# Optimization experiments

Hardware: AMD Instinct MI355X
Metric: run time of the kernel (lower is better)

The kernel has to match this reference:

```python
import jax, jax.numpy as jnp
import numpy as np

N, D, L = 1000, 256, 7  # nodes, feature dim, layers (hardcoded in the torch module)
B = 64


def setup_inputs() -> dict:
    key = jax.random.key(0)
    ks = jax.random.split(key, 8)
    x = jax.random.normal(ks[0], (B, N, D), dtype=jnp.float32)
    # binary adjacency mask (diagonal is forced to 1 inside reference, as in torch)
    adj = (jax.random.uniform(ks[1], (B, N, N)) < 0.05).astype(jnp.float32)
    # stacked per-layer weights; torch Linear convention: y = x @ W.T + b
    W_attn = jax.random.normal(ks[2], (L, D, D), dtype=jnp.float32) * 0.01
    b_attn = jnp.zeros((L, D), jnp.float32)
    W0 = jax.random.normal(ks[3], (L, D, D), dtype=jnp.float32) * 0.05
    b0 = jnp.zeros((L, D), jnp.float32)
    W1 = jax.random.normal(ks[4], (L, D, D), dtype=jnp.float32) * 0.05
    b1 = jnp.zeros((L, D), jnp.float32)
    Wf = jax.random.normal(ks[5], (D, D), dtype=jnp.float32) * 0.05
    bf = jnp.zeros((D,), jnp.float32)
    return {"x": x, "adj": adj, "W_attn": W_attn, "b_attn": b_attn,
            "W0": W0, "b0": b0, "W1": W1, "b1": b1, "Wf": Wf, "bf": bf}


def reference(x, adj, W_attn, b_attn, W0, b0, W1, b1, Wf, bf):
    idx = jnp.arange(N)
    adj = adj.at[:, idx, idx].set(1.0)              # self-loops forced on
    eps_eye = (1e-5 * jnp.eye(N, dtype=x.dtype))    # added before masking
    for l in range(L):
        x0 = x
        q = x @ W_attn[l].T + b_attn[l]             # [B,N,D]
        s = jax.nn.sigmoid(jnp.einsum('bid,bjd->bij', q, x))  # [B,N,N]
        s = (s + eps_eye) * adj                     # mask by adjacency
        s = s / jnp.sum(s, axis=-1, keepdims=True)  # row-sum normalize
        x = jnp.einsum('bij,bjd->bid', s, x)        # weighted aggregate
        x = jax.nn.relu(x @ W0[l].T + b0[l])
        x = jax.nn.relu(x @ W1[l].T + b1[l])
        x = x + x0                                  # residual
    return x @ Wf.T + bf
```

## Files before the change

kernel.cpp:

```cpp
#include <hip/hip_runtime.h>
#include <hip/hip_bf16.h>

#define B_ 64
#define N_ 1000
#define NP 1024
#define D_ 256
#define L_ 7
#define MP (B_*NP)
#define PKB 262144

typedef unsigned short u16;
typedef __attribute__((ext_vector_type(4))) float f32x4;
typedef __bf16 bf16x8 __attribute__((ext_vector_type(8)));

static __device__ __forceinline__ u16 f2bf(float f) {
  __hip_bfloat16 h = __float2bfloat16(f);
  return *reinterpret_cast<u16*>(&h);
}
static __device__ __forceinline__ float bf2f(u16 u) {
  __hip_bfloat16 h;
  *reinterpret_cast<u16*>(&h) = u;
  return __bfloat162float(h);
}

static __device__ __forceinline__ void gl_lds16(const u16* g, u16* l) {
  __builtin_amdgcn_global_load_lds(
      (const __attribute__((address_space(1))) void*)g,
      (__attribute__((address_space(3))) void*)l, 16, 0, 0);
}

__global__ __launch_bounds__(64) void pack_mask_k(const float* __restrict__ adj,
                                                  unsigned long long* __restrict__ mask) {
  int row = blockIdx.x;
  int b = row / N_, i = row - b * N_;
  int lane = threadIdx.x;
  const float* arow = adj + (size_t)(b * N_ + i) * N_;
  #pragma unroll
  for (int j0 = 0; j0 < NP; j0 += 64) {
    int j = j0 + lane;
    bool on = (j < N_) && (arow[j] != 0.0f || j == i);
    unsigned long long m = __ballot(on);
    if (lane == 0) mask[((size_t)(b * NP + i)) * 16 + (j0 >> 6)] = m;
  }
}

__global__ __launch_bounds__(256) void conv_w_k(const float* __restrict__ Wa,
                                                const float* __restrict__ W0,
                                                const float* __restrict__ W1,
                                                const float* __restrict__ Wf,
                                                u16* __restrict__ wpk) {
  int T = blockIdx.x * 256 + threadIdx.x;
  const int NW = 3 * L_ + 1;
  if (T >= NW * 128 * 64) return;
  int lane = T & 63;
  int fid = T >> 6;
  int k = fid & 7, f = (fid >> 3) & 3, by = (fid >> 5) & 3, w = fid >> 7;
  const float* src;
  if (w < L_) src = Wa + (size_t)w * D_ * D_;
  else if (w < 2 * L_) src = W0 + (size_t)(w - L_) * D_ * D_;
  else if (w < 3 * L_) src = W1 + (size_t)(w - 2 * L_) * D_ * D_;
  else src = Wf;
  int row = by * 64 + f * 16 + (lane & 15);
  int col = k * 32 + ((lane >> 4) << 3);
  const float* s = src + (size_t)row * D_ + col;
  u16 out8[8];
  #pragma unroll
  for (int e = 0; e < 8; e++) out8[e] = f2bf(s[e]);
  *reinterpret_cast<bf16x8*>(wpk + (size_t)T * 8) =
      *reinterpret_cast<bf16x8*>(out8);
}

__global__ __launch_bounds__(256) void prep_x_k(const float* __restrict__ x,
                                                float* __restrict__ xc,
                                                u16* __restrict__ xb) {
  size_t t = (size_t)blockIdx.x * blockDim.x + threadIdx.x;
  const size_t total = (size_t)B_ * N_ * D_;
  if (t < total) {
    int b = (int)(t / (N_ * D_));
    int rem = (int)(t - (size_t)b * (N_ * D_));
    size_t o = (size_t)b * NP * D_ + rem;
    float v = x[t];
    xc[o] = v;
    xb[o] = f2bf(v);
  }
  const size_t padTotal = (size_t)B_ * (NP - N_) * D_;
  if (t < padTotal) {
    int b = (int)(t / ((NP - N_) * D_));
    int rem = (int)(t - (size_t)b * ((NP - N_) * D_));
    size_t o = (size_t)b * NP * D_ + (size_t)N_ * D_ + rem;
    xc[o] = 0.f;
    xb[o] = 0;
  }
}

__global__ __launch_bounds__(256) void pack_both_k(const u16* __restrict__ xb,
                                                   u16* __restrict__ xpk,
                                                   u16* __restrict__ pvpk) {
  __shared__ u16 t[64][65];
  int b = blockIdx.z;
  int cc = blockIdx.x;
  int bd = blockIdx.y;
  int i0 = cc * 64, d0 = bd * 64;
  int tid = threadIdx.x;
  int tx = tid & 63, ty = tid >> 6;
  const u16* src = xb + (size_t)b * NP * D_;
  #pragma unroll
  for (int r = ty; r < 64; r += 4)
    t[r][tx] = src[(size_t)(i0 + r) * D_ + d0 + tx];
  __syncthreads();
  int lane = tid & 63, q = tid >> 6;
  int l4 = lane >> 4, l15 = lane & 15;
  int dh = bd >> 1, dcb = (bd & 1) * 4;
  u16* dstp = pvpk + (size_t)b * PKB;
  #pragma unroll
  for (int kk = 0; kk < 2; kk++) {
    int frag = cc * 32 + dh * 16 + (dcb + q) * 2 + kk;
    bf16x8 v;
    #pragma unroll
    for (int e = 0; e < 8; e++)
      v[e] = *reinterpret_cast<const __bf16*>(&t[kk * 32 + (l4 << 3) + e][q * 16 + l15]);
    *reinterpret_cast<bf16x8*>(dstp + (size_t)frag * 512 + lane * 8) = v;
  }
  u16* dstq = xpk + (size_t)b * PKB;
  #pragma unroll
  for (int kk = 0; kk < 2; kk++) {
    int frag = cc * 32 + q * 8 + (2 * bd + kk);
    bf16x8 v;
    #pragma unroll
    for (int e = 0; e < 8; e++)
      v[e] = *reinterpret_cast<const __bf16*>(&t[l15 + 16 * q][kk * 32 + (l4 << 3) + e]);
    *reinterpret_cast<bf16x8*>(dstq + (size_t)frag * 512 + lane * 8) = v;
  }
}

template <int MODE, int APK>
__global__ __launch_bounds__(256) void linear_k(const u16* __restrict__ A,
                                                const u16* __restrict__ W,
                                                const float* __restrict__ bias,
                                                u16* __restrict__ outb,
                                                float* __restrict__ xc,
                                                u16* __restrict__ xbp,
                                                float* __restrict__ outf) {
  int lane = threadIdx.x & 63;
  int wv = threadIdx.x >> 6;
  int rbase = blockIdx.x * 64 + wv * 16;
  int cbase = blockIdx.y * 64;
  f32x4 acc[4] = {};
  const u16* Ar;
  if (APK) Ar = A + ((size_t)(rbase >> 4) << 12) + lane * 8;
  else     Ar = A + (size_t)(rbase + (lane & 15)) * D_ + ((lane >> 4) << 3);
  const u16* Wr = W + (size_t)blockIdx.y * (32 * 512) + lane * 8;
  #pragma unroll
  for (int k = 0; k < 8; k++) {
    bf16x8 a = APK ? *reinterpret_cast<const bf16x8*>(Ar + k * 512)
                   : *reinterpret_cast<const bf16x8*>(Ar + k * 32);
    #pragma unroll
    for (int f = 0; f < 4; f++) {
      bf16x8 bb = *reinterpret_cast<const bf16x8*>(Wr + (f * 8 + k) * 512);
      acc[f] = __builtin_amdgcn_mfma_f32_16x16x32_bf16(a, bb, acc[f], 0, 0, 0);
    }
  }
  int r0 = rbase + ((lane >> 4) << 2);
  int col = cbase + (lane & 15);
  #pragma unroll
  for (int f = 0; f < 4; f++) {
    int c = col + f * 16;
    float bv = bias[c];
    #pragma unroll
    for (int r = 0; r < 4; r++) {
      int row = r0 + r;
      float v = acc[f][r] + bv;
      if (MODE == 3) {
        int b = row >> 10, i = row & (NP - 1);
        if (i < N_) outf[((size_t)b * N_ + i) * D_ + c] = v;
      } else {
        size_t dst = ((size_t)(row >> 4) << 12) + ((c >> 5) << 9) +
                     ((((c >> 3) & 3) * 16 + (row & 15)) << 3) + (c & 7);
        outb[dst] = f2bf(v);
      }
    }
  }
}

template <int FINAL>
__global__ __launch_bounds__(256) void mlp_fused_k(const u16* __restrict__ A,
                                                   const u16* __restrict__ W0p,
                                                   const float* __restrict__ bias0,
                                                   const u16* __restrict__ W1p,
                                                   const float* __restrict__ bias1,
                                                   u16* __restrict__ xpk,
                                                   float* __restrict__ xc,
                                                   u16* __restrict__ pvpk,
                                                   const u16* __restrict__ Wqp,
                                                   const float* __restrict__ biasq,
                                                   u16* __restrict__ qpk,
                                                   float* __restrict__ outf) {
  __shared__ u16 h0lds[8192];
  __shared__ u16 xnlds[8192];
  int blk = blockIdx.x;
  int lane = threadIdx.x & 63;
  int wv = threadIdx.x >> 6;
  int rsub = wv & 1, ch = wv >> 1;
  int l15 = lane & 15, l4 = lane >> 4;

  const u16* Ar = A + (size_t)(blk * 32 + rsub * 16 + l15) * D_ + (l4 << 3);
  const u16* w0b = W0p + (size_t)(ch * 64) * 512 + lane * 8;
  #pragma unroll
  for (int hf = 0; hf < 2; hf++) {
    f32x4 acc1[4] = {};
    __builtin_amdgcn_s_setprio(1);
    #pragma unroll
    for (int k = 0; k < 8; k++) {
      bf16x8 a = *reinterpret_cast<const bf16x8*>(Ar + k * 32);
      #pragma unroll
      for (int ff = 0; ff < 4; ff++) {
        bf16x8 bb = *reinterpret_cast<const bf16x8*>(
            w0b + (hf * 32 + ff * 8 + k) * 512);
        acc1[ff] = __builtin_amdgcn_mfma_f32_16x16x32_bf16(a, bb, acc1[ff], 0, 0, 0);
      }
    }
    __builtin_amdgcn_s_setprio(0);
    #pragma unroll
    for (int ff = 0; ff < 4; ff++) {
      int fc = hf * 4 + ff;
      int c = ch * 128 + fc * 16 + l15;
      float bv = bias0[c];
      int base = rsub * 4096 + (ch * 4 + (fc >> 1)) * 512 +
                 (((fc * 2 + (l15 >> 3)) & 3) * 16 + l4 * 4) * 8 + (l15 & 7);
      #pragma unroll
      for (int r = 0; r < 4; r++)
        h0lds[base + r * 8] = f2bf(fmaxf(acc1[ff][r] + bv, 0.f));
    }
  }
  __syncthreads();

  const u16* w1b = W1p + (size_t)(ch * 64) * 512 + lane * 8;
  int r0g = blk * 32 + rsub * 16 + l4 * 4;
  #pragma unroll
  for (int hf = 0; hf < 2; hf++) {
    f32x4 acc2[4] = {};
    __builtin_amdgcn_s_setprio(1);
    #pragma unroll
    for (int k = 0; k < 8; k++) {
      bf16x8 a = *reinterpret_cast<const bf16x8*>(&h0lds[rsub * 4096 + k * 512 + lane * 8]);
      #pragma unroll
      for (int ff = 0; ff < 4; ff++) {
        bf16x8 bb = *reinterpret_cast<const bf16x8*>(
            w1b + (hf * 32 + ff * 8 + k) * 512);
        acc2[ff] = __builtin_amdgcn_mfma_f32_16x16x32_bf16(a, bb, acc2[ff], 0, 0, 0);
      }
    }
    __builtin_amdgcn_s_setprio(0);
    #pragma unroll
    for (int ff = 0; ff < 4; ff++) {
      int fc = hf * 4 + ff;
      int c = ch * 128 + fc * 16 + l15;
      float bv = bias1[c];
      int base = rsub * 4096 + (ch * 4 + (fc >> 1)) * 512 +
                 (((fc * 2 + (l15 >> 3)) & 3) * 16 + l4 * 4) * 8 + (l15 & 7);
      #pragma unroll
      for (int r = 0; r < 4; r++) {
        int row = r0g + r;
        float v = fmaxf(acc2[ff][r] + bv, 0.f);
        size_t o = (size_t)row * D_ + c;
        float nv = v + xc[o];
        if (!FINAL) xc[o] = nv;
        xnlds[base + r * 8] = f2bf(nv);
      }
    }
  }
  __syncthreads();

  if (!FINAL) {
    int tid = threadIdx.x;
    u16* dst = xpk + ((size_t)blk << 13) + tid * 8;
    #pragma unroll
    for (int i = 0; i < 4; i++)
      *reinterpret_cast<bf16x8*>(dst + i * 2048) =
          *reinterpret_cast<const bf16x8*>(&xnlds[tid * 8 + i * 2048]);
    int rg = tid & 3;
    int cb = tid >> 2;
    int bb2 = blk >> 5;
    int fp_base = ((blk & 31) >> 1) * 32 + (blk & 1);
    #pragma unroll
    for (int pass = 0; pass < 4; pass++) {
      int c = pass * 64 + cb;
      int fragp = fp_base + (c >> 7) * 16 + ((c >> 4) & 7) * 2;
      size_t dp = (size_t)bb2 * PKB + (size_t)fragp * 512 +
                  (size_t)((rg * 16 + (c & 15)) << 3);
      int xoff = (rg >> 1) * 4096 + (c >> 5) * 512 +
                 ((((c >> 3) & 3) * 16 + (rg & 1) * 8) << 3) + (c & 7);
      u16 v[8];
      #pragma unroll
      for (int j = 0; j < 8; j++) v[j] = xnlds[xoff + j * 8];
      *reinterpret_cast<bf16x8*>(pvpk + dp) = *reinterpret_cast<bf16x8*>(v);
    }
  }

  const u16* wqb = Wqp + (size_t)(ch * 64) * 512 + lane * 8;
  #pragma unroll
  for (int hf = 0; hf < 2; hf++) {
    f32x4 acc3[4] = {};
    __builtin_amdgcn_s_setprio(1);
    #pragma unroll
    for (int k = 0; k < 8; k++) {
      bf16x8 a = *reinterpret_cast<const bf16x8*>(&xnlds[rsub * 4096 + k * 512 + lane * 8]);
      #pragma unroll
      for (int ff = 0; ff < 4; ff++) {
        bf16x8 bb = *reinterpret_cast<const bf16x8*>(
            wqb + (hf * 32 + ff * 8 + k) * 512);
        acc3[ff] = __builtin_amdgcn_mfma_f32_16x16x32_bf16(a, bb, acc3[ff], 0, 0, 0);
      }
    }
    __builtin_amdgcn_s_setprio(0);
    #pragma unroll
    for (int ff = 0; ff < 4; ff++) {
      int fc = hf * 4 + ff;
      int c = ch * 128 + fc * 16 + l15;
      float bv = biasq[c];
      #pragma unroll
      for (int r = 0; r < 4; r++) {
        int row = r0g + r;
        float v = acc3[ff][r] + bv;
        if (FINAL) {
          int b = row >> 10, i = row & (NP - 1);
          if (i < N_) outf[((size_t)b * N_ + i) * D_ + c] = v;
        } else {
          size_t dst = ((size_t)(row >> 4) << 12) + ((c >> 5) << 9) +
                       ((((c >> 3) & 3) * 16 + (row & 15)) << 3) + (c & 7);
          qpk[dst] = f2bf(v);
        }
      }
    }
  }
}

__global__ __launch_bounds__(512) void attn_fused_k(const u16* __restrict__ qpk,
                                                    const u16* __restrict__ xpk,
                                                    const u16* __restrict__ pvpk,
                                                    const unsigned long long* __restrict__ mask,
                                                    u16* __restrict__ yb) {
  __shared__ u16 xlds[16384];
  __shared__ u16 plds[2][64][64];
  __shared__ u16 qlds[16384];
  float* dlds = (float*)xlds;
  int wg = blockIdx.x;
  int xcd = wg & 7, slot = wg >> 3;
  int b = xcd * 8 + (slot >> 4);
  int rb = slot & 15;
  int rbase = rb * 64;
  int lane = threadIdx.x & 63;
  int wv = threadIdx.x >> 6;
  int rsub = wv & 3, jh = wv >> 2;
  int l15 = lane & 15, l4 = lane >> 4;
  int rowL = rsub * 16 + l4 * 4;

  const u16* xpkC = xpk + (size_t)b * PKB;
  const u16* pvkB = pvpk + (size_t)b * PKB + (size_t)((wv >> 2) * 16 + (wv & 3) * 4) * 512 + lane * 8;
  const unsigned long long* mB = mask + (size_t)b * (NP * 16);
  int swr = (l15 & 7) << 3;
  int pc0 = (l4 << 3) ^ swr;
  int pc1 = (32 | (l4 << 3)) ^ swr;

  f32x4 yacc[4][2] = {};
  float denp[4] = {0.f, 0.f, 0.f, 0.f};

  {
    const u16* gs = xpkC + wv * 2048 + lane * 8;
    u16* ld = &xlds[wv * 2048];
    #pragma unroll
    for (int i = 0; i < 4; i++)
      gl_lds16(gs + i * 512, ld + i * 512);
    const u16* gq = qpk + ((((size_t)b * NP + rbase) >> 4) << 12) + wv * 2048 + lane * 8;
    u16* lq = &qlds[wv * 2048];
    #pragma unroll
    for (int i = 0; i < 4; i++)
      gl_lds16(gq + i * 512, lq + i * 512);
  }
  __syncthreads();

  #pragma unroll 1
  for (int t = 0; t < 16; t++) {
    int pb = t & 1, pr = pb ^ 1;
    f32x4 sacc[2] = {};
    __builtin_amdgcn_s_setprio(1);
    #pragma unroll
    for (int k = 0; k < 8; k++) {
      bf16x8 a = *reinterpret_cast<const bf16x8*>(&qlds[rsub * 4096 + k * 512 + lane * 8]);
      bf16x8 b0 = *reinterpret_cast<const bf16x8*>(&xlds[((jh * 2) * 8 + k) * 512 + lane * 8]);
      sacc[0] = __builtin_amdgcn_mfma_f32_16x16x32_bf16(a, b0, sacc[0], 0, 0, 0);
      bf16x8 b1 = *reinterpret_cast<const bf16x8*>(&xlds[((jh * 2 + 1) * 8 + k) * 512 + lane * 8]);
      sacc[1] = __builtin_amdgcn_mfma_f32_16x16x32_bf16(a, b1, sacc[1], 0, 0, 0);
    }
    __builtin_amdgcn_s_setprio(0);
    __syncthreads();
    if (t < 15) {
      const u16* gs = xpkC + (size_t)(t + 1) * 16384 + wv * 2048 + lane * 8;
      u16* ld = &xlds[wv * 2048];
      #pragma unroll
      for (int i = 0; i < 4; i++)
        gl_lds16(gs + i * 512, ld + i * 512);
    }
    #pragma unroll
    for (int r = 0; r < 4; r++) {
      int i = rbase + rowL + r;
      unsigned long long mw = (i < N_) ? mB[((size_t)i << 4) + t] : 0ull;
      int swz = ((rowL + r) & 7) << 3;
      #pragma unroll
      for (int fl = 0; fl < 2; fl++) {
        int jloc = jh * 32 + fl * 16 + l15;
        int j = t * 64 + jloc;
        float w = 0.f;
        if ((mw >> jloc) & 1ull) {
          float s = __builtin_amdgcn_rcpf(1.f + __expf(-sacc[fl][r]));
          w = s + (i == j ? 1e-5f : 0.f);
        }
        u16 wq = f2bf(w);
        plds[pb][rowL + r][jloc ^ swz] = wq;
        denp[r] += bf2f(wq);
      }
    }
    if (t > 0) {
      const u16* pvc = pvkB + (size_t)(t - 1) * (32 * 512);
      bf16x8 w00 = *reinterpret_cast<const bf16x8*>(pvc);
      bf16x8 w01 = *reinterpret_cast<const bf16x8*>(pvc + 512);
      bf16x8 w10 = *reinterpret_cast<const bf16x8*>(pvc + 1024);
      bf16x8 w11 = *reinterpret_cast<const bf16x8*>(pvc + 1536);
      __builtin_amdgcn_s_setprio(1);
      #pragma unroll
      for (int rt = 0; rt < 4; rt++) {
        bf16x8 ap0 = *reinterpret_cast<const bf16x8*>(&plds[pr][rt * 16 + l15][pc0]);
        yacc[rt][0] = __builtin_amdgcn_mfma_f32_16x16x32_bf16(ap0, w00, yacc[rt][0], 0, 0, 0);
        yacc[rt][1] = __builtin_amdgcn_mfma_f32_16x16x32_bf16(ap0, w10, yacc[rt][1], 0, 0, 0);
        bf16x8 ap1 = *reinterpret_cast<const bf16x8*>(&plds[pr][rt * 16 + l15][pc1]);
        yacc[rt][0] = __builtin_amdgcn_mfma_f32_16x16x32_bf16(ap1, w01, yacc[rt][0], 0, 0, 0);
        yacc[rt][1] = __builtin_amdgcn_mfma_f32_16x16x32_bf16(ap1, w11, yacc[rt][1], 0, 0, 0);
      }
      __builtin_amdgcn_s_setprio(0);
    }
    __syncthreads();
  }

  {
    const u16* pvc = pvkB + (size_t)15 * (32 * 512);
    bf16x8 w00 = *reinterpret_cast<const bf16x8*>(pvc);
    bf16x8 w01 = *reinterpret_cast<const bf16x8*>(pvc + 512);
    bf16x8 w10 = *reinterpret_cast<const bf16x8*>(pvc + 1024);
    bf16x8 w11 = *reinterpret_cast<const bf16x8*>(pvc + 1536);
    __builtin_amdgcn_s_setprio(1);
    #pragma unroll
    for (int rt = 0; rt < 4; rt++) {
      bf16x8 ap0 = *reinterpret_cast<const bf16x8*>(&plds[1][rt * 16 + l15][pc0]);
      yacc[rt][0] = __builtin_amdgcn_mfma_f32_16x16x32_bf16(ap0, w00, yacc[rt][0], 0, 0, 0);
      yacc[rt][1] = __builtin_amdgcn_mfma_f32_16x16x32_bf16(ap0, w10, yacc[rt][1], 0, 0, 0);
      bf16x8 ap1 = *reinterpret_cast<const bf16x8*>(&plds[1][rt * 16 + l15][pc1]);
      yacc[rt][0] = __builtin_amdgcn_mfma_f32_16x16x32_bf16(ap1, w01, yacc[rt][0], 0, 0, 0);
      yacc[rt][1] = __builtin_amdgcn_mfma_f32_16x16x32_bf16(ap1, w11, yacc[rt][1], 0, 0, 0);
    }
    __builtin_amdgcn_s_setprio(0);
  }

  __syncthreads();
  #pragma unroll
  for (int r = 0; r < 4; r++) {
    float d = denp[r];
    #pragma unroll
    for (int m = 1; m < 16; m <<= 1) d += __shfl_xor(d, m, 64);
    if (l15 == 0) dlds[wv * 16 + l4 * 4 + r] = d;
  }
  __syncthreads();
  u16* yB = yb + ((size_t)b * NP + rbase) * D_ + wv * 32 + l15;
  #pragma unroll
  for (int rt = 0; rt < 4; rt++) {
    #pragma unroll
    for (int r = 0; r < 4; r++) {
      int rl = rt * 16 + l4 * 4 + r;
      int i = rbase + rl;
      float den = dlds[rt * 16 + l4 * 4 + r] + dlds[(rt + 4) * 16 + l4 * 4 + r];
      float inv = (i < N_ && den > 0.f) ? 1.f / den : 0.f;
      #pragma unroll
      for (int ct = 0; ct < 2; ct++)
        yB[(size_t)rl * D_ + ct * 16] = f2bf(yacc[rt][ct][r] * inv);
    }
  }
}

extern "C" void kernel_launch(void* const* d_in, const int* in_sizes, int n_in,
                              void* d_out, int out_size, void* d_ws, size_t ws_size,
                              hipStream_t stream) {
  const float* x   = (const float*)d_in[0];
  const float* adj = (const float*)d_in[1];
  const float* Wa  = (const float*)d_in[2];
  const float* ba  = (const float*)d_in[3];
  const float* W0  = (const float*)d_in[4];
  const float* b0_ = (const float*)d_in[5];
  const float* W1  = (const float*)d_in[6];
  const float* b1_ = (const float*)d_in[7];
  const float* Wf  = (const float*)d_in[8];
  const float* bff = (const float*)d_in[9];
  float* out = (float*)d_out;

  char* p = (char*)d_ws;
  auto alloc = [&](size_t bytes) {
    char* r = p;
    p += (bytes + 255) & ~(size_t)255;
    return r;
  };
  unsigned long long* mask = (unsigned long long*)alloc((size_t)B_ * NP * 16 * 8);
  u16* xb    = (u16*)alloc((size_t)MP * D_ * 2);
  u16* xpk   = (u16*)alloc((size_t)B_ * PKB * 2);
  u16* pvpk  = (u16*)alloc((size_t)B_ * PKB * 2);
  u16* qpk   = (u16*)alloc((size_t)MP * D_ * 2);
  u16* slotB = (u16*)alloc((size_t)MP * D_ * 2);
  float* xc  = (float*)alloc((size_t)MP * D_ * 4);
  u16* wb    = (u16*)alloc((size_t)(3 * L_ + 1) * D_ * D_ * 2);

  pack_mask_k<<<dim3(B_ * N_), dim3(64), 0, stream>>>(adj, mask);
  conv_w_k<<<dim3(704), dim3(256), 0, stream>>>(Wa, W0, W1, Wf, wb);
  prep_x_k<<<dim3((B_ * N_ * D_ + 255) / 256), dim3(256), 0, stream>>>(x, xc, xb);
  pack_both_k<<<dim3(16, 4, B_), dim3(256), 0, stream>>>(xb, xpk, pvpk);

  linear_k<4, 1><<<dim3(MP / 64, D_ / 64), dim3(256), 0, stream>>>(
      xpk, wb, ba, qpk, nullptr, nullptr, nullptr);

  for (int l = 0; l < L_; l++) {
    const u16* w0l = wb + (size_t)(L_ + l) * D_ * D_;
    const u16* w1l = wb + (size_t)(2 * L_ + l) * D_ * D_;

    attn_fused_k<<<dim3(1024), dim3(512), 0, stream>>>(
        qpk, xpk, pvpk, mask, slotB);
    if (l < L_ - 1) {
      mlp_fused_k<0><<<dim3(2048), dim3(256), 0, stream>>>(
          slotB, w0l, b0_ + l * D_, w1l, b1_ + l * D_, xpk, xc, pvpk,
          wb + (size_t)(l + 1) * D_ * D_, ba + (l + 1) * D_, qpk, nullptr);
    } else {
      mlp_fused_k<1><<<dim3(2048), dim3(256), 0, stream>>>(
          slotB, w0l, b0_ + l * D_, w1l, b1_ + l * D_, xpk, xc, pvpk,
          wb + (size_t)3 * L_ * D_ * D_, bff, nullptr, out);
    }
  }
}
```

Measured before the change: 1.588 ms.

## Drop separate transposed PV copy; read PV operand from staged x tile in LDS

Removes the second packed copy of x used as the B operand of the P·V matmul. The attention kernel now gathers those operands element-wise from the x tile already staged in LDS for the score matmul, using a swizzled staging offset. This saves global writes in the MLP kernel and global reads in attention. In exchange the P·V stage is no longer software-pipelined with double-buffered P, and the tile prefetch waits behind an extra barrier, so load latency may be less hidden. The 8-element scalar LDS gathers also add LDS traffic.

```diff
diff --git a/kernel.cpp b/kernel.cpp
--- a/kernel.cpp
+++ b/kernel.cpp
@@ -93,9 +93,8 @@
   }
 }
 
-__global__ __launch_bounds__(256) void pack_both_k(const u16* __restrict__ xb,
-                                                   u16* __restrict__ xpk,
-                                                   u16* __restrict__ pvpk) {
+__global__ __launch_bounds__(256) void pack_x_k(const u16* __restrict__ xb,
+                                                u16* __restrict__ xpk) {
   __shared__ u16 t[64][65];
   int b = blockIdx.z;
   int cc = blockIdx.x;
@@ -110,17 +109,6 @@
   __syncthreads();
   int lane = tid & 63, q = tid >> 6;
   int l4 = lane >> 4, l15 = lane & 15;
-  int dh = bd >> 1, dcb = (bd & 1) * 4;
-  u16* dstp = pvpk + (size_t)b * PKB;
-  #pragma unroll
-  for (int kk = 0; kk < 2; kk++) {
-    int frag = cc * 32 + dh * 16 + (dcb + q) * 2 + kk;
-    bf16x8 v;
-    #pragma unroll
-    for (int e = 0; e < 8; e++)
-      v[e] = *reinterpret_cast<const __bf16*>(&t[kk * 32 + (l4 << 3) + e][q * 16 + l15]);
-    *reinterpret_cast<bf16x8*>(dstp + (size_t)frag * 512 + lane * 8) = v;
-  }
   u16* dstq = xpk + (size_t)b * PKB;
   #pragma unroll
   for (int kk = 0; kk < 2; kk++) {
@@ -190,7 +178,6 @@
                                                    const float* __restrict__ bias1,
                                                    u16* __restrict__ xpk,
                                                    float* __restrict__ xc,
-                                                   u16* __restrict__ pvpk,
                                                    const u16* __restrict__ Wqp,
                                                    const float* __restrict__ biasq,
                                                    u16* __restrict__ qpk,
@@ -278,23 +265,6 @@
     for (int i = 0; i < 4; i++)
       *reinterpret_cast<bf16x8*>(dst + i * 2048) =
           *reinterpret_cast<const bf16x8*>(&xnlds[tid * 8 + i * 2048]);
-    int rg = tid & 3;
-    int cb = tid >> 2;
-    int bb2 = blk >> 5;
-    int fp_base = ((blk & 31) >> 1) * 32 + (blk & 1);
-    #pragma unroll
-    for (int pass = 0; pass < 4; pass++) {
-      int c = pass * 64 + cb;
-      int fragp = fp_base + (c >> 7) * 16 + ((c >> 4) & 7) * 2;
-      size_t dp = (size_t)bb2 * PKB + (size_t)fragp * 512 +
-                  (size_t)((rg * 16 + (c & 15)) << 3);
-      int xoff = (rg >> 1) * 4096 + (c >> 5) * 512 +
-                 ((((c >> 3) & 3) * 16 + (rg & 1) * 8) << 3) + (c & 7);
-      u16 v[8];
-      #pragma unroll
-      for (int j = 0; j < 8; j++) v[j] = xnlds[xoff + j * 8];
-      *reinterpret_cast<bf16x8*>(pvpk + dp) = *reinterpret_cast<bf16x8*>(v);
-    }
   }
 
   const u16* wqb = Wqp + (size_t)(ch * 64) * 512 + lane * 8;
@@ -337,12 +307,11 @@
 
 __global__ __launch_bounds__(512) void attn_fused_k(const u16* __restrict__ qpk,
                                                     const u16* __restrict__ xpk,
-                                                    const u16* __restrict__ pvpk,
                                                     const unsigned long long* __restrict__ mask,
                                                     u16* __restrict__ yb) {
   __shared__ u16 xlds[16384];
-  __shared__ u16 plds[2][64][64];
   __shared__ u16 qlds[16384];
+  __shared__ u16 plds[64][64];
   float* dlds = (float*)xlds;
   int wg = blockIdx.x;
   int xcd = wg & 7, slot = wg >> 3;
@@ -356,22 +325,29 @@
   int rowL = rsub * 16 + l4 * 4;
 
   const u16* xpkC = xpk + (size_t)b * PKB;
-  const u16* pvkB = pvpk + (size_t)b * PKB + (size_t)((wv >> 2) * 16 + (wv & 3) * 4) * 512 + lane * 8;
   const unsigned long long* mB = mask + (size_t)b * (NP * 16);
   int swr = (l15 & 7) << 3;
   int pc0 = (l4 << 3) ^ swr;
   int pc1 = (32 | (l4 << 3)) ^ swr;
+  int loff = 8 * (lane ^ (lane >> 3));
+  int pvb = ((lane >> 5) & 1) * 4096 + (wv >> 1) * 1024 + (wv & 1) * 512 +
+            ((lane & 15) >> 3) * 128 + ((lane >> 4) & 1) * 64 + (lane & 7);
+  int x3 = ((lane >> 4) & 1) | (((lane & 15) >> 3) << 1);
+  int G00 = pvb + (x3 << 3);
+  int G01 = pvb + 256 + ((x3 ^ 4) << 3);
+  int G10 = G00 + 8192;
+  int G11 = G01 + 8192;
 
   f32x4 yacc[4][2] = {};
   float denp[4] = {0.f, 0.f, 0.f, 0.f};
 
   {
-    const u16* gs = xpkC + wv * 2048 + lane * 8;
+    const u16* gs = xpkC + wv * 2048 + loff;
     u16* ld = &xlds[wv * 2048];
     #pragma unroll
     for (int i = 0; i < 4; i++)
       gl_lds16(gs + i * 512, ld + i * 512);
-    const u16* gq = qpk + ((((size_t)b * NP + rbase) >> 4) << 12) + wv * 2048 + lane * 8;
+    const u16* gq = qpk + ((((size_t)b * NP + rbase) >> 4) << 12) + wv * 2048 + loff;
     u16* lq = &qlds[wv * 2048];
     #pragma unroll
     for (int i = 0; i < 4; i++)
@@ -381,26 +357,17 @@
 
   #pragma unroll 1
   for (int t = 0; t < 16; t++) {
-    int pb = t & 1, pr = pb ^ 1;
     f32x4 sacc[2] = {};
     __builtin_amdgcn_s_setprio(1);
     #pragma unroll
     for (int k = 0; k < 8; k++) {
-      bf16x8 a = *reinterpret_cast<const bf16x8*>(&qlds[rsub * 4096 + k * 512 + lane * 8]);
-      bf16x8 b0 = *reinterpret_cast<const bf16x8*>(&xlds[((jh * 2) * 8 + k) * 512 + lane * 8]);
+      bf16x8 a = *reinterpret_cast<const bf16x8*>(&qlds[rsub * 4096 + k * 512 + loff]);
+      bf16x8 b0 = *reinterpret_cast<const bf16x8*>(&xlds[(16 * jh + k) * 512 + loff]);
       sacc[0] = __builtin_amdgcn_mfma_f32_16x16x32_bf16(a, b0, sacc[0], 0, 0, 0);
-      bf16x8 b1 = *reinterpret_cast<const bf16x8*>(&xlds[((jh * 2 + 1) * 8 + k) * 512 + lane * 8]);
+      bf16x8 b1 = *reinterpret_cast<const bf16x8*>(&xlds[(16 * jh + 8 + k) * 512 + loff]);
       sacc[1] = __builtin_amdgcn_mfma_f32_16x16x32_bf16(a, b1, sacc[1], 0, 0, 0);
     }
     __builtin_amdgcn_s_setprio(0);
-    __syncthreads();
-    if (t < 15) {
-      const u16* gs = xpkC + (size_t)(t + 1) * 16384 + wv * 2048 + lane * 8;
-      u16* ld = &xlds[wv * 2048];
-      #pragma unroll
-      for (int i = 0; i < 4; i++)
-        gl_lds16(gs + i * 512, ld + i * 512);
-    }
     #pragma unroll
     for (int r = 0; r < 4; r++) {
       int i = rbase + rowL + r;
@@ -416,51 +383,50 @@
           w = s + (i == j ? 1e-5f : 0.f);
         }
         u16 wq = f2bf(w);
-        plds[pb][rowL + r][jloc ^ swz] = wq;
+        plds[rowL + r][jloc ^ swz] = wq;
         denp[r] += bf2f(wq);
       }
     }
-    if (t > 0) {
-      const u16* pvc = pvkB + (size_t)(t - 1) * (32 * 512);
-      bf16x8 w00 = *reinterpret_cast<const bf16x8*>(pvc);
-      bf16x8 w01 = *reinterpret_cast<const bf16x8*>(pvc + 512);
-      bf16x8 w10 = *reinterpret_cast<const bf16x8*>(pvc + 1024);
-      bf16x8 w11 = *reinterpret_cast<const bf16x8*>(pvc + 1536);
+    __syncthreads();
+    {
+      const __bf16* xb16 = reinterpret_cast<const __bf16*>(xlds);
       __builtin_amdgcn_s_setprio(1);
+      bf16x8 w0, w1;
+      #pragma unroll
+      for (int e = 0; e < 8; e++) {
+        w0[e] = xb16[G00 ^ (e * 8)];
+        w1[e] = xb16[G01 ^ (e * 8)];
+      }
       #pragma unroll
       for (int rt = 0; rt < 4; rt++) {
-        bf16x8 ap0 = *reinterpret_cast<const bf16x8*>(&plds[pr][rt * 16 + l15][pc0]);
-        yacc[rt][0] = __builtin_amdgcn_mfma_f32_16x16x32_bf16(ap0, w00, yacc[rt][0], 0, 0, 0);
-        yacc[rt][1] = __builtin_amdgcn_mfma_f32_16x16x32_bf16(ap0, w10, yacc[rt][1], 0, 0, 0);
-        bf16x8 ap1 = *reinterpret_cast<const bf16x8*>(&plds[pr][rt * 16 + l15][pc1]);
-        yacc[rt][0] = __builtin_amdgcn_mfma_f32_16x16x32_bf16(ap1, w01, yacc[rt][0], 0, 0, 0);
-        yacc[rt][1] = __builtin_amdgcn_mfma_f32_16x16x32_bf16(ap1, w11, yacc[rt][1], 0, 0, 0);
+        bf16x8 ap = *reinterpret_cast<const bf16x8*>(&plds[rt * 16 + l15][pc0]);
+        yacc[rt][0] = __builtin_amdgcn_mfma_f32_16x16x32_bf16(ap, w0, yacc[rt][0], 0, 0, 0);
+        yacc[rt][1] = __builtin_amdgcn_mfma_f32_16x16x32_bf16(ap, w1, yacc[rt][1], 0, 0, 0);
+      }
+      #pragma unroll
+      for (int e = 0; e < 8; e++) {
+        w0[e] = xb16[G10 ^ (e * 8)];
+        w1[e] = xb16[G11 ^ (e * 8)];
+      }
+      #pragma unroll
+      for (int rt = 0; rt < 4; rt++) {
+        bf16x8 ap = *reinterpret_cast<const bf16x8*>(&plds[rt * 16 + l15][pc1]);
+        yacc[rt][0] = __builtin_amdgcn_mfma_f32_16x16x32_bf16(ap, w0, yacc[rt][0], 0, 0, 0);
+        yacc[rt][1] = __builtin_amdgcn_mfma_f32_16x16x32_bf16(ap, w1, yacc[rt][1], 0, 0, 0);
       }
       __builtin_amdgcn_s_setprio(0);
     }
     __syncthreads();
-  }
-
-  {
-    const u16* pvc = pvkB + (size_t)15 * (32 * 512);
-    bf16x8 w00 = *reinterpret_cast<const bf16x8*>(pvc);
-    bf16x8 w01 = *reinterpret_cast<const bf16x8*>(pvc + 512);
-    bf16x8 w10 = *reinterpret_cast<const bf16x8*>(pvc + 1024);
-    bf16x8 w11 = *reinterpret_cast<const bf16x8*>(pvc + 1536);
-    __builtin_amdgcn_s_setprio(1);
-    #pragma unroll
-    for (int rt = 0; rt < 4; rt++) {
-      bf16x8 ap0 = *reinterpret_cast<const bf16x8*>(&plds[1][rt * 16 + l15][pc0]);
-      yacc[rt][0] = __builtin_amdgcn_mfma_f32_16x16x32_bf16(ap0, w00, yacc[rt][0], 0, 0, 0);
-      yacc[rt][1] = __builtin_amdgcn_mfma_f32_16x16x32_bf16(ap0, w10, yacc[rt][1], 0, 0, 0);
-      bf16x8 ap1 = *reinterpret_cast<const bf16x8*>(&plds[1][rt * 16 + l15][pc1]);
-      yacc[rt][0] = __builtin_amdgcn_mfma_f32_16x16x32_bf16(ap1, w01, yacc[rt][0], 0, 0, 0);
-      yacc[rt][1] = __builtin_amdgcn_mfma_f32_16x16x32_bf16(ap1, w11, yacc[rt][1], 0, 0, 0);
-    }
-    __builtin_amdgcn_s_setprio(0);
-  }
-
-  __syncthreads();
+    if (t < 15) {
+      const u16* gs = xpkC + (size_t)(t + 1) * 16384 + wv * 2048 + loff;
+      u16* ld = &xlds[wv * 2048];
+      #pragma unroll
+      for (int i = 0; i < 4; i++)
+        gl_lds16(gs + i * 512, ld + i * 512);
+    }
+    __syncthreads();
+  }
+
   #pragma unroll
   for (int r = 0; r < 4; r++) {
     float d = denp[r];
@@ -509,7 +475,6 @@
   unsigned long long* mask = (unsigned long long*)alloc((size_t)B_ * NP * 16 * 8);
   u16* xb    = (u16*)alloc((size_t)MP * D_ * 2);
   u16* xpk   = (u16*)alloc((size_t)B_ * PKB * 2);
-  u16* pvpk  = (u16*)alloc((size_t)B_ * PKB * 2);
   u16* qpk   = (u16*)alloc((size_t)MP * D_ * 2);
   u16* slotB = (u16*)alloc((size_t)MP * D_ * 2);
   float* xc  = (float*)alloc((size_t)MP * D_ * 4);
@@ -518,7 +483,7 @@
   pack_mask_k<<<dim3(B_ * N_), dim3(64), 0, stream>>>(adj, mask);
   conv_w_k<<<dim3(704), dim3(256), 0, stream>>>(Wa, W0, W1, Wf, wb);
   prep_x_k<<<dim3((B_ * N_ * D_ + 255) / 256), dim3(256), 0, stream>>>(x, xc, xb);
-  pack_both_k<<<dim3(16, 4, B_), dim3(256), 0, stream>>>(xb, xpk, pvpk);
+  pack_x_k<<<dim3(16, 4, B_), dim3(256), 0, stream>>>(xb, xpk);
 
   linear_k<4, 1><<<dim3(MP / 64, D_ / 64), dim3(256), 0, stream>>>(
       xpk, wb, ba, qpk, nullptr, nullptr, nullptr);
@@ -528,14 +493,14 @@
     const u16* w1l = wb + (size_t)(2 * L_ + l) * D_ * D_;
 
     attn_fused_k<<<dim3(1024), dim3(512), 0, stream>>>(
-        qpk, xpk, pvpk, mask, slotB);
+        qpk, xpk, mask, slotB);
     if (l < L_ - 1) {
       mlp_fused_k<0><<<dim3(2048), dim3(256), 0, stream>>>(
-          slotB, w0l, b0_ + l * D_, w1l, b1_ + l * D_, xpk, xc, pvpk,
+          slotB, w0l, b0_ + l * D_, w1l, b1_ + l * D_, xpk, xc,
           wb + (size_t)(l + 1) * D_ * D_, ba + (l + 1) * D_, qpk, nullptr);
     } else {
       mlp_fused_k<1><<<dim3(2048), dim3(256), 0, stream>>>(
-          slotB, w0l, b0_ + l * D_, w1l, b1_ + l * D_, xpk, xc, pvpk,
+          slotB, w0l, b0_ + l * D_, w1l, b1_ + l * D_, xpk, xc,
           wb + (size_t)3 * L_ * D_ * D_, bff, nullptr, out);
     }
   }
```

Result: faster. 1.555 ms (median of 2 runs) (-2.1%).
